# Performance work log

Measured on AMD Instinct MI355X. Metric: run time of the kernel, lower is better.

The kernel has to match this reference:

```python
import jax, jax.numpy as jnp
import numpy as np

DIM = 1024
NUM_HEADS = 16
HEAD_DIM = DIM // NUM_HEADS
ROPE_BASE = 10000.0


def _rope_cos_sin(seq_len, head_dim, dtype):
    inv_freq = 1.0 / (ROPE_BASE ** (jnp.arange(0, head_dim, 2, dtype=jnp.float32) / head_dim))
    t = jnp.arange(seq_len, dtype=jnp.float32)
    freqs = jnp.einsum('i,j->ij', t, inv_freq)          # (S, head_dim/2)
    emb = jnp.concatenate([freqs, freqs], axis=-1)       # (S, head_dim)
    return jnp.cos(emb).astype(dtype), jnp.sin(emb).astype(dtype)


def _rotate_half(x):
    x1, x2 = jnp.split(x, 2, axis=-1)
    return jnp.concatenate([-x2, x1], axis=-1)


def setup_inputs() -> dict:
    key = jax.random.key(0)
    k1, k2, k3 = jax.random.split(key, 3)
    B, S = 2, 2048
    x = jax.random.normal(k1, (B, S, DIM), dtype=jnp.float32)
    w_qkv = jax.random.normal(k2, (3 * DIM, DIM), dtype=jnp.float32) * (DIM ** -0.5)
    w_out = jax.random.normal(k3, (DIM, DIM), dtype=jnp.float32) * (DIM ** -0.5)
    return {"x": x, "w_qkv": w_qkv, "w_out": w_out}


def reference(x, w_qkv, w_out):
    B, S, _ = x.shape
    scale = HEAD_DIM ** -0.5

    qkv = jnp.einsum('bsd,ed->bse', x, w_qkv)                 # (B, S, 3*DIM)
    qkv = qkv.reshape(B, S, 3, NUM_HEADS, HEAD_DIM)
    qkv = jnp.transpose(qkv, (2, 0, 3, 1, 4))                  # (3, B, H, S, hd)
    Q, K, V = qkv[0], qkv[1], qkv[2]

    cos, sin = _rope_cos_sin(S, HEAD_DIM, x.dtype)             # (S, hd)
    Q = Q * cos + _rotate_half(Q) * sin
    K = K * cos + _rotate_half(K) * sin

    scores = jnp.einsum('bhqd,bhkd->bhqk', Q, K) * scale       # (B, H, S, S)
    causal = jnp.tril(jnp.ones((S, S), dtype=bool))
    scores = jnp.where(causal[None, None], scores, jnp.asarray(-1e9, scores.dtype))
    attn = jax.nn.softmax(scores, axis=-1)

    out = jnp.einsum('bhqk,bhkd->bhqd', attn, V)               # (B, H, S, hd)
    out = jnp.transpose(out, (0, 2, 1, 3)).reshape(B, S, DIM)
    out = jnp.einsum('bsd,ed->bse', out, w_out)
    return out
```

## Files before the change

kernel.cpp:

```cpp
#include <hip/hip_runtime.h>
#include <hip/hip_bf16.h>

#define DIM 1024
#define NHEADS 16
#define HD 64
#define BB 2
#define SS 2048
#define MTOT (BB*SS)
#define SCALE 0.125f
#define QSCALE 0.1803368801111204f

typedef __attribute__((ext_vector_type(8))) short bf16x8;
typedef __attribute__((ext_vector_type(4))) float f32x4;

__device__ __forceinline__ float bf2f(short u) {
  union { float f; unsigned int i; } v;
  v.i = ((unsigned int)(unsigned short)u) << 16;
  return v.f;
}
__device__ __forceinline__ short f2bf(float f) {
  union { float f; unsigned int i; } v; v.f = f;
  unsigned int r = v.i + 0x7fffu + ((v.i >> 16) & 1u);
  return (short)(r >> 16);
}
__device__ __forceinline__ unsigned int cvtpk_bf16(float lo, float hi) {
  unsigned int r;
  asm("v_cvt_pk_bf16_f32 %0, %1, %2" : "=v"(r) : "v"(lo), "v"(hi));
  return r;
}
__device__ __forceinline__ void async_load16(const short* g, short* l) {
  __builtin_amdgcn_global_load_lds(
      (const __attribute__((address_space(1))) unsigned int*)g,
      (__attribute__((address_space(3))) unsigned int*)l, 16, 0, 0);
}

__global__ void cvt3_kernel(const float* __restrict__ a, short* __restrict__ oa, int na,
                            const float* __restrict__ b, short* __restrict__ ob, int nb,
                            const float* __restrict__ c, short* __restrict__ oc, int nc,
                            float* __restrict__ ct, float* __restrict__ st) {
  int gid = blockIdx.x * blockDim.x + threadIdx.x;
  if (gid < SS * 32) {
    int s = gid >> 5, j = gid & 31;
    float inv = 1.0f / powf(10000.0f, (float)(2 * j) / 64.0f);
    float ang = (float)s * inv;
    ct[gid] = cosf(ang);
    st[gid] = sinf(ang);
  }
  int stride = gridDim.x * blockDim.x;
  int tot = na + nb + nc;
  for (int q = gid; q < tot; q += stride) {
    const float* src; short* dst; int off;
    if (q < na)            { src = a; dst = oa; off = q; }
    else if (q < na + nb)  { src = b; dst = ob; off = q - na; }
    else                   { src = c; dst = oc; off = q - na - nb; }
    float4 v = *(const float4*)(src + (size_t)off * 4);
    short4 o;
    o.x = f2bf(v.x); o.y = f2bf(v.y); o.z = f2bf(v.z); o.w = f2bf(v.w);
    *(short4*)(dst + (size_t)off * 4) = o;
  }
}

template<bool OUT_F32>
__global__ __launch_bounds__(256) void gemm_bt(
    const short* __restrict__ A, const short* __restrict__ B,
    void* __restrict__ C, int M, int N, int K) {
  __shared__ __align__(16) short As[128][32];
  __shared__ __align__(16) short Bs[128][32];
  const int nbx = N >> 7;
  const int chunk = gridDim.x >> 3;
  const int wg = (blockIdx.x & 7) * chunk + (blockIdx.x >> 3);
  const int m0 = (wg / nbx) * 128, n0 = (wg % nbx) * 128;
  const int tid = threadIdx.x;
  const int lane = tid & 63;
  const int wid = tid >> 6;
  const int wm = (wid >> 1) * 64, wn = (wid & 1) * 64;
  const int row = lane & 15, kg = (lane >> 4) * 8;
  const int lrow = lane >> 2;
  const int lcol = (lane & 3) * 8;

  f32x4 acc[4][4];
#pragma unroll
  for (int m = 0; m < 4; m++)
#pragma unroll
    for (int n = 0; n < 4; n++) acc[m][n] = (f32x4){0.f, 0.f, 0.f, 0.f};

  for (int kk = 0; kk < K; kk += 32) {
    __syncthreads();
#pragma unroll
    for (int i = 0; i < 2; i++) {
      int base = i * 64 + wid * 16;
      async_load16(A + (size_t)(m0 + base + lrow) * K + kk + lcol, &As[base][0]);
      async_load16(B + (size_t)(n0 + base + lrow) * K + kk + lcol, &Bs[base][0]);
    }
    __syncthreads();
    bf16x8 af[4], bfr[4];
#pragma unroll
    for (int m = 0; m < 4; m++) af[m] = *(const bf16x8*)(&As[wm + m * 16 + row][kg]);
#pragma unroll
    for (int n = 0; n < 4; n++) bfr[n] = *(const bf16x8*)(&Bs[wn + n * 16 + row][kg]);
#pragma unroll
    for (int m = 0; m < 4; m++)
#pragma unroll
      for (int n = 0; n < 4; n++)
        acc[m][n] = __builtin_amdgcn_mfma_f32_16x16x32_bf16(af[m], bfr[n], acc[m][n], 0, 0, 0);
  }
  const int orow = (lane >> 4) * 4, ocol = lane & 15;
#pragma unroll
  for (int m = 0; m < 4; m++)
#pragma unroll
    for (int n = 0; n < 4; n++)
#pragma unroll
      for (int r = 0; r < 4; r++) {
        int gr = m0 + wm + m * 16 + orow + r;
        int gc = n0 + wn + n * 16 + ocol;
        if (OUT_F32) ((float*)C)[(size_t)gr * N + gc] = acc[m][n][r];
        else         ((short*)C)[(size_t)gr * N + gc] = f2bf(acc[m][n][r]);
      }
}

__global__ __launch_bounds__(256) void ropev_kernel(
    const short* __restrict__ qkv, const float* __restrict__ ct, const float* __restrict__ st,
    short* __restrict__ Q, short* __restrict__ K, short* __restrict__ Vt) {
  int bh = blockIdx.y;
  int b = bh >> 4, h = bh & 15;
  int t = threadIdx.x;
  if (blockIdx.x < SS / 64) {
    int s0 = blockIdx.x * 64;
    int rl = t >> 2;
    int d8 = (t & 3) * 8;
    int s = s0 + rl;
    size_t inbase = ((size_t)(b * SS + s)) * 3072 + h * 64 + d8;
    size_t outbase = ((size_t)bh * SS + s) * 64;
    float c[8], sn[8];
#pragma unroll
    for (int j = 0; j < 8; j++) { c[j] = ct[s * 32 + d8 + j]; sn[j] = st[s * 32 + d8 + j]; }
    {
      bf16x8 x1 = *(const bf16x8*)(qkv + inbase);
      bf16x8 x2 = *(const bf16x8*)(qkv + inbase + 32);
      bf16x8 o1, o2;
#pragma unroll
      for (int j = 0; j < 8; j++) {
        float a = bf2f(x1[j]), bb = bf2f(x2[j]);
        o1[j] = f2bf((a * c[j] - bb * sn[j]) * QSCALE);
        o2[j] = f2bf((bb * c[j] + a * sn[j]) * QSCALE);
      }
      *(bf16x8*)(Q + outbase + d8) = o1;
      *(bf16x8*)(Q + outbase + d8 + 32) = o2;
    }
    {
      bf16x8 x1 = *(const bf16x8*)(qkv + inbase + 1024);
      bf16x8 x2 = *(const bf16x8*)(qkv + inbase + 1024 + 32);
      bf16x8 o1, o2;
#pragma unroll
      for (int j = 0; j < 8; j++) {
        float a = bf2f(x1[j]), bb = bf2f(x2[j]);
        o1[j] = f2bf(a * c[j] - bb * sn[j]);
        o2[j] = f2bf(bb * c[j] + a * sn[j]);
      }
      int pc = (t & 3) ^ (s & 7);
      *(bf16x8*)(K + outbase + pc * 8) = o1;
      *(bf16x8*)(K + outbase + (pc ^ 4) * 8) = o2;
    }
  } else {
    __shared__ short ls[64][72];
    int s0 = (blockIdx.x - SS / 64) * 64;
#pragma unroll
    for (int p = 0; p < 2; p++) {
      int idx = p * 256 + t;
      int r = idx >> 3, c8 = (idx & 7) * 8;
      *(bf16x8*)(&ls[r][c8]) =
          *(const bf16x8*)(qkv + ((size_t)(b * SS + s0 + r)) * 3072 + 2048 + h * 64 + c8);
    }
    __syncthreads();
    int dl = t >> 2, sg = (t & 3) * 16;
    int c = sg >> 5, hi = (sg >> 4) & 1;
    short tmp[16];
#pragma unroll
    for (int j = 0; j < 16; j++) tmp[j] = ls[sg + j][dl];
    size_t rowbase = ((size_t)bh * 64 + dl) * SS + s0;
#pragma unroll
    for (int g = 0; g < 4; g++) {
      short4 o = { tmp[4 * g], tmp[4 * g + 1], tmp[4 * g + 2], tmp[4 * g + 3] };
      int pc = (c * 4 + g) ^ (dl & 7);
      *(short4*)(Vt + rowbase + pc * 8 + hi * 4) = o;
    }
  }
}

__global__ __launch_bounds__(256, 6) void attn_kernel(
    const short* __restrict__ Qp, const short* __restrict__ Kp, const short* __restrict__ Vt,
    short* __restrict__ O, float* __restrict__ Pf) {
  __shared__ __align__(16) short KsF[64 * 64];
  __shared__ __align__(16) short VsF[64 * 64];
  int flat = blockIdx.x;
  int wk = (flat & 7) * 128 + (flat >> 3);
  int bh = wk >> 5;
  int sub = wk & 31;
  int pr = sub >> 1, half = sub & 1;
  int b = bh >> 4, h = bh & 15;
  int tid = threadIdx.x, lane = tid & 63, w = tid >> 6;
  int row = lane & 15, grp = lane >> 4;
  const int qtH = 31 - pr;
  const int nseg = 1 + half;
  const int ck = (grp ^ (row & 7)) * 8;

  const short* Kbase = Kp + (size_t)bh * SS * 64;
  const short* Vbase = Vt + (size_t)bh * 64 * SS;
  const int sr8 = lane >> 3;
  const int sc8 = (lane & 7) * 8;

  const int kts0 = half ? 16 : 0;

#pragma unroll 1
  for (int s = 0; s < nseg; s++) {
    const int qt  = (s == 0) ? qtH : pr;
    const int kts = (s == 0) ? kts0 : 0;
    const int kte = (s == 0) ? (half ? qtH : 15) : pr;
    const bool fin = (s == 1);
    const int q0 = qt * 64;
    const int q = q0 + w * 16 + row;
    bf16x8 qf0, qf1;
    {
      size_t qb = ((size_t)bh * SS + q) * 64 + grp * 8;
      qf0 = *(const bf16x8*)(Qp + qb);
      qf1 = *(const bf16x8*)(Qp + qb + 32);
    }
    f32x4 acc[4];
#pragma unroll
    for (int d = 0; d < 4; d++) acc[d] = (f32x4){0.f, 0.f, 0.f, 0.f};
    float m = -1e30f, l = 0.f;

#pragma unroll 1
    for (int kt = kts; kt <= kte; kt++) {
      int kv0 = kt * 64;
      __syncthreads();
#pragma unroll
      for (int i = 0; i < 2; i++) {
        int rbase = i * 32 + w * 8;
        async_load16(Kbase + (size_t)(kv0 + rbase + sr8) * 64 + sc8, &KsF[rbase * 64]);
        async_load16(Vbase + (size_t)(rbase + sr8) * SS + kv0 + sc8, &VsF[rbase * 64]);
      }
      __syncthreads();

      bool last = (kt == qt);
      float sv[4][4];
      __builtin_amdgcn_s_setprio(1);
#pragma unroll
      for (int n = 0; n < 4; n++) {
        if (last && n > w) {
#pragma unroll
          for (int r = 0; r < 4; r++) sv[n][r] = -1e30f;
          continue;
        }
        f32x4 sf = (f32x4){0.f, 0.f, 0.f, 0.f};
        const short* kr_ = &KsF[(n * 16 + row) * 64];
        bf16x8 kf0 = *(const bf16x8*)(kr_ + ck);
        bf16x8 kf1 = *(const bf16x8*)(kr_ + (ck ^ 32));
        sf = __builtin_amdgcn_mfma_f32_16x16x32_bf16(kf0, qf0, sf, 0, 0, 0);
        sf = __builtin_amdgcn_mfma_f32_16x16x32_bf16(kf1, qf1, sf, 0, 0, 0);
#pragma unroll
        for (int r = 0; r < 4; r++) sv[n][r] = sf[r];
      }
      __builtin_amdgcn_s_setprio(0);
      if (last) {
#pragma unroll
        for (int n = 0; n < 4; n++)
#pragma unroll
          for (int r = 0; r < 4; r++) {
            int kv = kv0 + n * 16 + grp * 4 + r;
            if (kv > q) sv[n][r] = -1e30f;
          }
      }
      float pmax = -1e30f;
#pragma unroll
      for (int n = 0; n < 4; n++)
#pragma unroll
        for (int r = 0; r < 4; r++) pmax = fmaxf(pmax, sv[n][r]);
      pmax = fmaxf(pmax, __shfl_xor(pmax, 16));
      pmax = fmaxf(pmax, __shfl_xor(pmax, 32));
      if (__any(pmax - m > 8.f)) {
        float mnew = fmaxf(m, pmax);
        float resc = __builtin_amdgcn_exp2f(m - mnew);
        m = mnew;
        l *= resc;
#pragma unroll
        for (int d = 0; d < 4; d++)
#pragma unroll
          for (int r = 0; r < 4; r++) acc[d][r] *= resc;
      }
      float psum = 0.f;
#pragma unroll
      for (int n = 0; n < 4; n++)
#pragma unroll
        for (int r = 0; r < 4; r++) {
          float pv = __builtin_amdgcn_exp2f(sv[n][r] - m);
          sv[n][r] = pv;
          psum += pv;
        }
      psum += __shfl_xor(psum, 16);
      psum += __shfl_xor(psum, 32);
      l += psum;
      __builtin_amdgcn_s_setprio(1);
#pragma unroll
      for (int c = 0; c < 2; c++) {
        union { unsigned int u[4]; bf16x8 v; } pu;
        pu.u[0] = cvtpk_bf16(sv[2 * c][0], sv[2 * c][1]);
        pu.u[1] = cvtpk_bf16(sv[2 * c][2], sv[2 * c][3]);
        pu.u[2] = cvtpk_bf16(sv[2 * c + 1][0], sv[2 * c + 1][1]);
        pu.u[3] = cvtpk_bf16(sv[2 * c + 1][2], sv[2 * c + 1][3]);
#pragma unroll
        for (int dm = 0; dm < 4; dm++) {
          const short* vr_ = &VsF[(dm * 16 + row) * 64];
          bf16x8 vf = *(const bf16x8*)(vr_ + (ck ^ (c * 32)));
          acc[dm] = __builtin_amdgcn_mfma_f32_16x16x32_bf16(vf, pu.v, acc[dm], 0, 0, 0);
        }
      }
      __builtin_amdgcn_s_setprio(0);
    }
    if (fin) {
      float linv = 1.0f / l;
      size_t ob = ((size_t)(b * SS + q)) * 1024 + h * 64 + grp * 4;
#pragma unroll
      for (int dm = 0; dm < 4; dm++) {
        union { unsigned int u[2]; short4 s4; } ou;
        ou.u[0] = cvtpk_bf16(acc[dm][0] * linv, acc[dm][1] * linv);
        ou.u[1] = cvtpk_bf16(acc[dm][2] * linv, acc[dm][3] * linv);
        *(short4*)(O + ob + dm * 16) = ou.s4;
      }
    } else {
      int slot = (bh * 16 + (qt - 16)) * 2 + half;
      float* P = Pf + (size_t)slot * 64 * 68 + (w * 16 + row) * 68;
#pragma unroll
      for (int dm = 0; dm < 4; dm++) {
        f32x4 a = acc[dm];
        *(float4*)(P + dm * 16 + grp * 4) = *(float4*)&a;
      }
      if (grp == 0) { P[64] = m; P[65] = l; }
    }
  }
}

__global__ __launch_bounds__(64) void merge_kernel(const float* __restrict__ Pf, short* __restrict__ O) {
  int bh = blockIdx.x >> 4, ht = blockIdx.x & 15;
  int b = bh >> 4, h = bh & 15;
  int qt = ht + 16;
  int t = threadIdx.x;
  const float* p0 = Pf + ((size_t)((bh * 16 + ht) * 2)) * 64 * 68 + t * 68;
  const float* p1 = p0 + 64 * 68;
  float m0 = p0[64], l0 = p0[65], m1 = p1[64], l1 = p1[65];
  float mM = fmaxf(m0, m1);
  float e0 = __builtin_amdgcn_exp2f(m0 - mM);
  float e1 = __builtin_amdgcn_exp2f(m1 - mM);
  float linv = 1.0f / (e0 * l0 + e1 * l1);
  size_t ob = ((size_t)(b * SS + qt * 64 + t)) * 1024 + h * 64;
#pragma unroll
  for (int d8 = 0; d8 < 8; d8++) {
    float4 a0 = *(const float4*)(p0 + d8 * 8);
    float4 a1 = *(const float4*)(p1 + d8 * 8);
    float4 b0 = *(const float4*)(p0 + d8 * 8 + 4);
    float4 b1 = *(const float4*)(p1 + d8 * 8 + 4);
    union { unsigned int u[4]; short4 s4[2]; } ou;
    ou.u[0] = cvtpk_bf16((e0 * a0.x + e1 * a1.x) * linv, (e0 * a0.y + e1 * a1.y) * linv);
    ou.u[1] = cvtpk_bf16((e0 * a0.z + e1 * a1.z) * linv, (e0 * a0.w + e1 * a1.w) * linv);
    ou.u[2] = cvtpk_bf16((e0 * b0.x + e1 * b1.x) * linv, (e0 * b0.y + e1 * b1.y) * linv);
    ou.u[3] = cvtpk_bf16((e0 * b0.z + e1 * b1.z) * linv, (e0 * b0.w + e1 * b1.w) * linv);
    *(short4*)(O + ob + d8 * 8) = ou.s4[0];
    *(short4*)(O + ob + d8 * 8 + 4) = ou.s4[1];
  }
}

extern "C" void kernel_launch(void* const* d_in, const int* in_sizes, int n_in,
                              void* d_out, int out_size, void* d_ws, size_t ws_size,
                              hipStream_t stream) {
  (void)in_sizes; (void)n_in; (void)out_size; (void)ws_size;
  const float* x     = (const float*)d_in[0];
  const float* w_qkv = (const float*)d_in[1];
  const float* w_out = (const float*)d_in[2];
  float* out = (float*)d_out;

  char* ws = (char*)d_ws;
  size_t off = 0;
  auto alloc = [&](size_t bytes) -> void* {
    void* p = ws + off;
    off += (bytes + 255) & ~(size_t)255;
    return p;
  };
  short* xb    = (short*)alloc((size_t)MTOT * DIM * 2);
  short* wqkvb = (short*)alloc((size_t)3072 * 1024 * 2);
  short* woutb = (short*)alloc((size_t)1024 * 1024 * 2);
  short* qkvb  = (short*)alloc((size_t)MTOT * 3072 * 2);
  short* Qb    = (short*)alloc((size_t)32 * SS * 64 * 2);
  short* Kb    = (short*)alloc((size_t)32 * SS * 64 * 2);
  short* Vtb   = (short*)alloc((size_t)32 * 64 * SS * 2);
  float* ct    = (float*)alloc((size_t)SS * 32 * 4);
  float* st    = (float*)alloc((size_t)SS * 32 * 4);
  short* attnb = xb;
  float* Pf    = (float*)qkvb;

  cvt3_kernel<<<2048, 256, 0, stream>>>(x, xb, MTOT * DIM / 4,
                                        w_qkv, wqkvb, 3072 * 1024 / 4,
                                        w_out, woutb, 1024 * 1024 / 4, ct, st);
  gemm_bt<false><<<(3072 / 128) * (MTOT / 128), 256, 0, stream>>>(xb, wqkvb, qkvb, MTOT, 3072, 1024);
  ropev_kernel<<<dim3(2 * SS / 64, 32), 256, 0, stream>>>(qkvb, ct, st, Qb, Kb, Vtb);
  attn_kernel<<<1024, 256, 0, stream>>>(Qb, Kb, Vtb, attnb, Pf);
  merge_kernel<<<512, 64, 0, stream>>>(Pf, attnb);
  gemm_bt<true><<<(1024 / 128) * (MTOT / 128), 256, 0, stream>>>(attnb, woutb, out, MTOT, 1024, 1024);
}
```

Measured before the change: 130.3 us.

## Double-buffer K/V tiles in attention and use narrower tiles for output GEMM

The attention kernel now double-buffers its K and V shared-memory tiles. It issues async loads for the next tile, including the first tile of the next segment, before computing on the current one, with explicit vmcnt waits and barriers. This is meant to hide global-load latency behind the MFMA work. Separately, the output projection GEMM uses a 128x64 tile, which doubles its block count to improve occupancy and load balance for the small N=1024 case. The costs are twice the attention LDS footprint, which may lower occupancy under launch_bounds 6, and a second barrier per iteration.

```diff
diff --git a/kernel.cpp b/kernel.cpp
--- a/kernel.cpp
+++ b/kernel.cpp
@@ -60,29 +60,30 @@
   }
 }
 
-template<bool OUT_F32>
+template<int BN, bool OUT_F32>
 __global__ __launch_bounds__(256) void gemm_bt(
     const short* __restrict__ A, const short* __restrict__ B,
     void* __restrict__ C, int M, int N, int K) {
+  constexpr int NFR = BN / 32;
   __shared__ __align__(16) short As[128][32];
-  __shared__ __align__(16) short Bs[128][32];
-  const int nbx = N >> 7;
+  __shared__ __align__(16) short Bs[BN][32];
+  const int nbx = N / BN;
   const int chunk = gridDim.x >> 3;
   const int wg = (blockIdx.x & 7) * chunk + (blockIdx.x >> 3);
-  const int m0 = (wg / nbx) * 128, n0 = (wg % nbx) * 128;
+  const int m0 = (wg / nbx) * 128, n0 = (wg % nbx) * BN;
   const int tid = threadIdx.x;
   const int lane = tid & 63;
   const int wid = tid >> 6;
-  const int wm = (wid >> 1) * 64, wn = (wid & 1) * 64;
+  const int wm = (wid >> 1) * 64, wn = (wid & 1) * (BN / 2);
   const int row = lane & 15, kg = (lane >> 4) * 8;
   const int lrow = lane >> 2;
   const int lcol = (lane & 3) * 8;
 
-  f32x4 acc[4][4];
+  f32x4 acc[4][NFR];
 #pragma unroll
   for (int m = 0; m < 4; m++)
 #pragma unroll
-    for (int n = 0; n < 4; n++) acc[m][n] = (f32x4){0.f, 0.f, 0.f, 0.f};
+    for (int n = 0; n < NFR; n++) acc[m][n] = (f32x4){0.f, 0.f, 0.f, 0.f};
 
   for (int kk = 0; kk < K; kk += 32) {
     __syncthreads();
@@ -90,25 +91,34 @@
     for (int i = 0; i < 2; i++) {
       int base = i * 64 + wid * 16;
       async_load16(A + (size_t)(m0 + base + lrow) * K + kk + lcol, &As[base][0]);
+    }
+    if constexpr (BN == 128) {
+#pragma unroll
+      for (int i = 0; i < 2; i++) {
+        int base = i * 64 + wid * 16;
+        async_load16(B + (size_t)(n0 + base + lrow) * K + kk + lcol, &Bs[base][0]);
+      }
+    } else {
+      int base = wid * 16;
       async_load16(B + (size_t)(n0 + base + lrow) * K + kk + lcol, &Bs[base][0]);
     }
     __syncthreads();
-    bf16x8 af[4], bfr[4];
+    bf16x8 af[4], bfr[NFR];
 #pragma unroll
     for (int m = 0; m < 4; m++) af[m] = *(const bf16x8*)(&As[wm + m * 16 + row][kg]);
 #pragma unroll
-    for (int n = 0; n < 4; n++) bfr[n] = *(const bf16x8*)(&Bs[wn + n * 16 + row][kg]);
+    for (int n = 0; n < NFR; n++) bfr[n] = *(const bf16x8*)(&Bs[wn + n * 16 + row][kg]);
 #pragma unroll
     for (int m = 0; m < 4; m++)
 #pragma unroll
-      for (int n = 0; n < 4; n++)
+      for (int n = 0; n < NFR; n++)
         acc[m][n] = __builtin_amdgcn_mfma_f32_16x16x32_bf16(af[m], bfr[n], acc[m][n], 0, 0, 0);
   }
   const int orow = (lane >> 4) * 4, ocol = lane & 15;
 #pragma unroll
   for (int m = 0; m < 4; m++)
 #pragma unroll
-    for (int n = 0; n < 4; n++)
+    for (int n = 0; n < NFR; n++)
 #pragma unroll
       for (int r = 0; r < 4; r++) {
         int gr = m0 + wm + m * 16 + orow + r;
@@ -190,8 +200,8 @@
 __global__ __launch_bounds__(256, 6) void attn_kernel(
     const short* __restrict__ Qp, const short* __restrict__ Kp, const short* __restrict__ Vt,
     short* __restrict__ O, float* __restrict__ Pf) {
-  __shared__ __align__(16) short KsF[64 * 64];
-  __shared__ __align__(16) short VsF[64 * 64];
+  __shared__ __align__(16) short KsF[2][64 * 64];
+  __shared__ __align__(16) short VsF[2][64 * 64];
   int flat = blockIdx.x;
   int wk = (flat & 7) * 128 + (flat >> 3);
   int bh = wk >> 5;
@@ -209,7 +219,18 @@
   const int sr8 = lane >> 3;
   const int sc8 = (lane & 7) * 8;
 
+  auto STAGE = [&](int bufi, int kv0) {
+#pragma unroll
+    for (int i = 0; i < 2; i++) {
+      int rbase = i * 32 + w * 8;
+      async_load16(Kbase + (size_t)(kv0 + rbase + sr8) * 64 + sc8, &KsF[bufi][rbase * 64]);
+      async_load16(Vbase + (size_t)(rbase + sr8) * SS + kv0 + sc8, &VsF[bufi][rbase * 64]);
+    }
+  };
+
   const int kts0 = half ? 16 : 0;
+  int cur = 0;
+  STAGE(0, kts0 * 64);
 
 #pragma unroll 1
   for (int s = 0; s < nseg; s++) {
@@ -233,14 +254,18 @@
 #pragma unroll 1
     for (int kt = kts; kt <= kte; kt++) {
       int kv0 = kt * 64;
-      __syncthreads();
-#pragma unroll
-      for (int i = 0; i < 2; i++) {
-        int rbase = i * 32 + w * 8;
-        async_load16(Kbase + (size_t)(kv0 + rbase + sr8) * 64 + sc8, &KsF[rbase * 64]);
-        async_load16(Vbase + (size_t)(rbase + sr8) * SS + kv0 + sc8, &VsF[rbase * 64]);
-      }
-      __syncthreads();
+      bool more = (kt < kte) || (s + 1 < nseg);
+      if (more) {
+        STAGE(cur ^ 1, kt < kte ? kv0 + 64 : 0);
+        asm volatile("s_waitcnt vmcnt(4)" ::: "memory");
+      } else {
+        asm volatile("s_waitcnt vmcnt(0)" ::: "memory");
+      }
+      __builtin_amdgcn_sched_barrier(0);
+      __builtin_amdgcn_s_barrier();
+      __builtin_amdgcn_sched_barrier(0);
+      const short* Kc = &KsF[cur][0];
+      const short* Vc = &VsF[cur][0];
 
       bool last = (kt == qt);
       float sv[4][4];
@@ -253,7 +278,7 @@
           continue;
         }
         f32x4 sf = (f32x4){0.f, 0.f, 0.f, 0.f};
-        const short* kr_ = &KsF[(n * 16 + row) * 64];
+        const short* kr_ = Kc + (n * 16 + row) * 64;
         bf16x8 kf0 = *(const bf16x8*)(kr_ + ck);
         bf16x8 kf1 = *(const bf16x8*)(kr_ + (ck ^ 32));
         sf = __builtin_amdgcn_mfma_f32_16x16x32_bf16(kf0, qf0, sf, 0, 0, 0);
@@ -310,12 +335,16 @@
         pu.u[3] = cvtpk_bf16(sv[2 * c + 1][2], sv[2 * c + 1][3]);
 #pragma unroll
         for (int dm = 0; dm < 4; dm++) {
-          const short* vr_ = &VsF[(dm * 16 + row) * 64];
+          const short* vr_ = Vc + (dm * 16 + row) * 64;
           bf16x8 vf = *(const bf16x8*)(vr_ + (ck ^ (c * 32)));
           acc[dm] = __builtin_amdgcn_mfma_f32_16x16x32_bf16(vf, pu.v, acc[dm], 0, 0, 0);
         }
       }
       __builtin_amdgcn_s_setprio(0);
+      __builtin_amdgcn_sched_barrier(0);
+      __builtin_amdgcn_s_barrier();
+      __builtin_amdgcn_sched_barrier(0);
+      cur ^= 1;
     }
     if (fin) {
       float linv = 1.0f / l;
@@ -400,9 +429,9 @@
   cvt3_kernel<<<2048, 256, 0, stream>>>(x, xb, MTOT * DIM / 4,
                                         w_qkv, wqkvb, 3072 * 1024 / 4,
                                         w_out, woutb, 1024 * 1024 / 4, ct, st);
-  gemm_bt<false><<<(3072 / 128) * (MTOT / 128), 256, 0, stream>>>(xb, wqkvb, qkvb, MTOT, 3072, 1024);
+  gemm_bt<128, false><<<(3072 / 128) * (MTOT / 128), 256, 0, stream>>>(xb, wqkvb, qkvb, MTOT, 3072, 1024);
   ropev_kernel<<<dim3(2 * SS / 64, 32), 256, 0, stream>>>(qkvb, ct, st, Qb, Kb, Vtb);
   attn_kernel<<<1024, 256, 0, stream>>>(Qb, Kb, Vtb, attnb, Pf);
   merge_kernel<<<512, 64, 0, stream>>>(Pf, attnb);
-  gemm_bt<true><<<(1024 / 128) * (MTOT / 128), 256, 0, stream>>>(attnb, woutb, out, MTOT, 1024, 1024);
-}
+  gemm_bt<64, true><<<(1024 / 64) * (MTOT / 128), 256, 0, stream>>>(attnb, woutb, out, MTOT, 1024, 1024);
+}
```

New measurement: 128.8 us. No clear change (-1.1%).
